# Kernel optimization log

Hardware: AMD Instinct MI355X
Metric: run time of the kernel (lower is better)

The kernel has to match this reference:

```python
import jax, jax.numpy as jnp
import numpy as np

B, S, D, DH = 4, 2048, 1024, 64


def setup_inputs() -> dict:
    key = jax.random.key(0)
    ks = jax.random.split(key, 7)
    x = jax.random.normal(ks[0], (B, S, D), dtype=jnp.float32)
    def w(k):
        return jax.random.normal(k, (D, DH), dtype=jnp.float32) / np.sqrt(D).astype(np.float32)
    return {
        'x': x,
        'w_q_u': w(ks[1]), 'w_k_u': w(ks[2]), 'w_v_u': w(ks[3]),
        'w_q_c': w(ks[4]), 'w_k_c': w(ks[5]), 'w_v_c': w(ks[6]),
    }


def reference(x, w_q_u, w_k_u, w_v_u, w_q_c, w_k_c, w_v_c):
    b, n, _ = x.shape
    scale = w_q_u.shape[-1] ** -0.5
    # projections (LinearNoBias -> plain matmul)
    Q_u = x @ w_q_u
    K_u = x @ w_k_u
    V_u = x @ w_v_u
    Q_c = x @ w_q_c
    K_c = x @ w_k_c
    V_c = x @ w_v_c

    i = jnp.arange(n)
    causal = i[:, None] >= i[None, :]        # True where j <= i (binary causal / keep for S_c)
    lookahead = i[:, None] < i[None, :]      # True where j > i (allowed in sigmoid term)

    # term1: [b, n, n], zeroed above the diagonal via binary causal mask
    term1 = jnp.einsum('bid,bjd->bij', Q_c, V_u) * scale * causal.astype(x.dtype)

    # sigmoid gate: lookahead mask adds -inf on/below the diagonal -> sigmoid = 0 there
    logits_u = jnp.einsum('bid,bjd->bij', Q_u, K_u) * scale
    sigmoid_term = jax.nn.sigmoid(jnp.where(lookahead, logits_u, -jnp.inf))

    # nested n^3 matmul: S_u[b,i,k] = sum_j term1[b,i,j] * sigmoid_term[b,k,j]
    S_u = jnp.einsum('bij,bkj->bik', term1, sigmoid_term)

    S_c = jnp.where(causal, jnp.einsum('bid,bjd->bij', Q_c, K_c) * scale, -jnp.inf)

    attn = jax.nn.softmax(S_c - jax.nn.silu(S_u), axis=-1)
    return jnp.einsum('bij,bjd->bid', attn, V_c)
```

## Files before the change

kernel.cpp:

```cpp
#include <hip/hip_runtime.h>
#include <hip/hip_bf16.h>

typedef short bf16x8 __attribute__((ext_vector_type(8)));
typedef float f32x4  __attribute__((ext_vector_type(4)));
typedef _Float16 f16x8 __attribute__((ext_vector_type(8)));

#define MFMA16(a,b,c)  __builtin_amdgcn_mfma_f32_16x16x32_bf16((a),(b),(c),0,0,0)
#define MFMAF16(a,b,c) __builtin_amdgcn_mfma_f32_16x16x32_f16((a),(b),(c),0,0,0)

#define GLDS16(g,l) __builtin_amdgcn_global_load_lds( \
    (const __attribute__((address_space(1))) void*)(g), \
    (__attribute__((address_space(3))) void*)(l), 16, 0, 0)

__device__ __forceinline__ short f2bf(float f){
  union { float f; unsigned u; } v; v.f = f;
  unsigned r = v.u + 0x7fffu + ((v.u >> 16) & 1u);
  return (short)(r >> 16);
}
__device__ __forceinline__ float bf2f(short h){
  union { unsigned u; float f; } v; v.u = ((unsigned)(unsigned short)h) << 16;
  return v.f;
}
__device__ __forceinline__ void split8v(f32x4 a, f32x4 b, bf16x8& h, bf16x8& l){
  float t[8] = {a[0],a[1],a[2],a[3],b[0],b[1],b[2],b[3]};
  #pragma unroll
  for (int e = 0; e < 8; ++e){
    short hs = f2bf(t[e]);
    h[e] = hs;
    l[e] = f2bf(t[e] - bf2f(hs));
  }
}

__global__ void k_prep(const float* w0, const float* w1, const float* w2,
                       const float* w3, const float* w4, const float* w5,
                       const float* __restrict__ x,
                       unsigned short* __restrict__ wth, unsigned short* __restrict__ wtl,
                       unsigned short* __restrict__ xh, unsigned short* __restrict__ xl){
  int gb = blockIdx.x;
  if (gb < 1536){
    int p = gb >> 8;
    const float* wp = p==0?w0:p==1?w1:p==2?w2:p==3?w3:p==4?w4:w5;
    int idx = (gb & 255)*256 + threadIdx.x;
    int n = idx >> 10, k = idx & 1023;
    float v = wp[k*64 + n];
    short hs = f2bf(v);
    wth[(size_t)p*65536 + n*1024 + k] = (unsigned short)hs;
    wtl[(size_t)p*65536 + n*1024 + k] = (unsigned short)f2bf(v - bf2f(hs));
  } else {
    size_t i = ((size_t)(gb - 1536)*256 + threadIdx.x)*8;
    f32x4 a = *(const f32x4*)(x + i);
    f32x4 b = *(const f32x4*)(x + i + 4);
    bf16x8 h, l;
    split8v(a, b, h, l);
    *(bf16x8*)(xh + i) = h;
    *(bf16x8*)(xl + i) = l;
  }
}

__global__ __launch_bounds__(256) void k_proj(
    const unsigned short* __restrict__ xh, const unsigned short* __restrict__ xl,
    const unsigned short* __restrict__ wth, const unsigned short* __restrict__ wtl,
    unsigned short* __restrict__ projh, unsigned short* __restrict__ projl,
    _Float16* __restrict__ vct, _Float16* __restrict__ vuth, _Float16* __restrict__ vutl){
  __shared__ __align__(16) char sm[49152];
  int blk = blockIdx.x;
  int rb = blk/3, pg = blk - rb*3;
  int tid = threadIdx.x, w = tid >> 6, lane = tid & 63;
  int lm = lane & 15, quad = lane >> 4;
  int srow = lane >> 3, scg = (lane & 7) ^ srow;
  const char* xhg = (const char*)xh;
  const char* xlg = (const char*)xl;
  const char* w0h = (const char*)wth + (size_t)(pg*2  )*131072;
  const char* w0l = (const char*)wtl + (size_t)(pg*2  )*131072;
  const char* w1h = (const char*)wth + (size_t)(pg*2+1)*131072;
  const char* w1l = (const char*)wtl + (size_t)(pg*2+1)*131072;
  f32x4 acc[2][4] = {};
  for (int k0 = 0; k0 < 1024; k0 += 64){
    __syncthreads();
    size_t cb = (size_t)k0*2 + scg*16;
    #pragma unroll
    for (int i2 = 0; i2 < 2; ++i2){
      int i = w*2 + i2;
      size_t gx = (size_t)(rb*64 + i*8 + srow)*2048 + cb;
      size_t gw = (size_t)(i*8 + srow)*2048 + cb;
      GLDS16(xhg + gx, sm +         i*1024);
      GLDS16(xlg + gx, sm +  8192 + i*1024);
      GLDS16(w0h + gw, sm + 16384 + i*1024);
      GLDS16(w0l + gw, sm + 24576 + i*1024);
      GLDS16(w1h + gw, sm + 32768 + i*1024);
      GLDS16(w1l + gw, sm + 40960 + i*1024);
    }
    __syncthreads();
    #pragma unroll
    for (int ks = 0; ks < 2; ++ks){
      int ra = w*16 + lm;
      int offa = ra*128 + (((ks*4+quad) ^ (ra&7))*16);
      bf16x8 ah = *(const bf16x8*)(sm + offa);
      bf16x8 al = *(const bf16x8*)(sm + 8192 + offa);
      #pragma unroll
      for (int sub = 0; sub < 2; ++sub){
        #pragma unroll
        for (int n = 0; n < 4; ++n){
          int r = n*16 + lm;
          int off = r*128 + (((ks*4+quad) ^ (r&7))*16);
          bf16x8 bh = *(const bf16x8*)(sm + 16384 + sub*16384 + off);
          bf16x8 bl = *(const bf16x8*)(sm + 24576 + sub*16384 + off);
          acc[sub][n] = MFMA16(ah, bh, acc[sub][n]);
          acc[sub][n] = MFMA16(ah, bl, acc[sub][n]);
          acc[sub][n] = MFMA16(al, bh, acc[sub][n]);
        }
      }
    }
  }
  #pragma unroll
  for (int sub = 0; sub < 2; ++sub){
    int p = pg*2 + sub;
    if (p != 5){
      unsigned short* oph = projh + (size_t)p*524288;
      unsigned short* opl = projl + (size_t)p*524288;
      #pragma unroll
      for (int n = 0; n < 4; ++n)
        #pragma unroll
        for (int e = 0; e < 4; ++e){
          int r = rb*64 + w*16 + quad*4 + e;
          float f = acc[sub][n][e];
          short hs = f2bf(f);
          oph[(size_t)r*64 + n*16 + lm] = (unsigned short)hs;
          opl[(size_t)r*64 + n*16 + lm] = (unsigned short)f2bf(f - bf2f(hs));
        }
    }
  }
  if (pg == 1 || pg == 2){
    int sub = (pg == 1) ? 0 : 1;
    float (*T)[65] = (float (*)[65])sm;
    __syncthreads();
    #pragma unroll
    for (int n = 0; n < 4; ++n)
      #pragma unroll
      for (int e = 0; e < 4; ++e)
        T[w*16 + quad*4 + e][n*16 + lm] = acc[sub][n][e];
    __syncthreads();
    int b2 = rb >> 5, sl = (rb & 31)*64;
    int d = tid >> 2, sp = (tid & 3)*16;
    size_t o = (size_t)b2*131072 + (size_t)d*2048 + sl + sp;
    if (sub == 1){
      f16x8 h0, h1;
      #pragma unroll
      for (int j = 0; j < 8; ++j) h0[j] = (_Float16)T[sp + j][d];
      #pragma unroll
      for (int j = 0; j < 8; ++j) h1[j] = (_Float16)T[sp + 8 + j][d];
      *(f16x8*)(vct + o) = h0; *(f16x8*)(vct + o + 8) = h1;
    } else {
      f16x8 h0, h1, l0, l1;
      #pragma unroll
      for (int j = 0; j < 8; ++j){
        float f = T[sp + j][d];
        _Float16 h = (_Float16)f;
        h0[j] = h; l0[j] = (_Float16)(f - (float)h);
      }
      #pragma unroll
      for (int j = 0; j < 8; ++j){
        float f = T[sp + 8 + j][d];
        _Float16 h = (_Float16)f;
        h1[j] = h; l1[j] = (_Float16)(f - (float)h);
      }
      *(f16x8*)(vuth + o) = h0; *(f16x8*)(vuth + o + 8) = h1;
      *(f16x8*)(vutl + o) = l0; *(f16x8*)(vutl + o + 8) = l1;
    }
  }
}

__global__ __launch_bounds__(256,3) void k_p2(
    const unsigned short* __restrict__ ph, const unsigned short* __restrict__ pl,
    const _Float16* __restrict__ vuth, const _Float16* __restrict__ vutl,
    _Float16* __restrict__ sg, _Float16* __restrict__ t1d, float* __restrict__ W){
  __shared__ __align__(16) char sm[32768];
  int b = blockIdx.y;
  int t = blockIdx.x;
  bool isSig = t < 136;
  int a = 0, bb = 0;
  if (isSig){
    #pragma unroll 1
    for (int aa = 0; aa < 16; ++aa){
      int c = 16 - aa;
      if (t < c){ a = aa; bb = aa + t; break; }
      t -= c;
    }
  } else {
    a = bb = t - 136;
  }
  int pa = isSig ? 0 : 3;
  int pb = isSig ? 1 : 2;
  const char* Ahg = (const char*)ph + (size_t)pa*1048576;
  const char* Alg = (const char*)pl + (size_t)pa*1048576;
  const char* Bhg = (const char*)ph + (size_t)pb*1048576;
  const char* Blg = (const char*)pl + (size_t)pb*1048576;
  int tid = threadIdx.x, w = tid >> 6, lane = tid & 63;
  int lm = lane & 15, quad = lane >> 4;
  int wm = (w & 1)*64, wn = (w >> 1)*64;
  f32x4 acc[4][4] = {};
  #pragma unroll
  for (int ks = 0; ks < 2; ++ks){
    bf16x8 bh[4], bl[4];
    #pragma unroll
    for (int n = 0; n < 4; ++n){
      size_t off = (size_t)(b*2048 + bb*128 + wn + n*16 + lm)*128 + (ks*32 + quad*8)*2;
      bh[n] = *(const bf16x8*)(Bhg + off);
      bl[n] = *(const bf16x8*)(Blg + off);
    }
    #pragma unroll
    for (int m = 0; m < 4; ++m){
      size_t off = (size_t)(b*2048 + a*128 + wm + m*16 + lm)*128 + (ks*32 + quad*8)*2;
      bf16x8 ah = *(const bf16x8*)(Ahg + off);
      bf16x8 al = *(const bf16x8*)(Alg + off);
      #pragma unroll
      for (int n = 0; n < 4; ++n){
        acc[m][n] = MFMA16(ah, bh[n], acc[m][n]);
        acc[m][n] = MFMA16(ah, bl[n], acc[m][n]);
        acc[m][n] = MFMA16(al, bh[n], acc[m][n]);
      }
    }
  }
  #pragma unroll
  for (int m = 0; m < 4; ++m){
    #pragma unroll
    for (int n = 0; n < 4; ++n){
      #pragma unroll
      for (int e = 0; e < 4; ++e){
        int il = wm + m*16 + quad*4 + e;
        int jl = wn + n*16 + lm;
        int gi = a*128 + il, gj = bb*128 + jl;
        float v = acc[m][n][e];
        float outv;
        if (isSig) outv = (gj >  gi) ? (1.0f/(1.0f + __expf(-v*0.125f))) : 0.0f;
        else       outv = (gj <= gi) ? v : 0.0f;
        *(_Float16*)(sm + ((il*256 + jl*2) ^ ((il & 7) << 4))) = (_Float16)outv;
      }
    }
  }
  __syncthreads();
  char* outp = isSig
    ? (char*)(sg + (size_t)b*4194304 + (size_t)(a*128)*2048 + bb*128)
    : (char*)t1d + (size_t)(b*16 + a)*32768;
  size_t rstride = isSig ? 4096 : 256;
  #pragma unroll
  for (int r = 0; r < 8; ++r){
    int lrow = w*32 + r*4 + (lane >> 4);
    int c16 = lane & 15;
    f32x4 vv = *(const f32x4*)(sm + ((lrow*256 + c16*16) ^ ((lrow & 7) << 4)));
    *(f32x4*)(outp + (size_t)lrow*rstride + c16*16) = vv;
  }
  if (isSig){
    int wm2 = (w & 1)*64, wn2 = (w >> 1)*32;
    f32x4 acc2[4][2] = {};
    #pragma unroll
    for (int ks = 0; ks < 4; ++ks){
      f16x8 bh2[2], bl2[2];
      #pragma unroll
      for (int n = 0; n < 2; ++n){
        int d = wn2 + n*16 + lm;
        size_t jo = ((size_t)(b*64 + d)*2048 + bb*128 + ks*32 + quad*8)*2;
        bh2[n] = *(const f16x8*)((const char*)vuth + jo);
        bl2[n] = *(const f16x8*)((const char*)vutl + jo);
      }
      #pragma unroll
      for (int m = 0; m < 4; ++m){
        int k = wm2 + m*16 + lm;
        f16x8 af = *(const f16x8*)(sm + ((k*256 + ks*64 + quad*16) ^ ((k & 7) << 4)));
        #pragma unroll
        for (int n = 0; n < 2; ++n){
          acc2[m][n] = MFMAF16(af, bh2[n], acc2[m][n]);
          acc2[m][n] = MFMAF16(af, bl2[n], acc2[m][n]);
        }
      }
    }
    float* Wp = W + (size_t)(b*136 + bb*(bb+1)/2 + a)*8192;
    #pragma unroll
    for (int m = 0; m < 4; ++m)
      #pragma unroll
      for (int n = 0; n < 2; ++n)
        #pragma unroll
        for (int e = 0; e < 4; ++e){
          int r = wm2 + m*16 + quad*4 + e;
          int col = wn2 + n*16 + lm;
          Wp[r*64 + col] = acc2[m][n][e];
        }
  }
}

__global__ __launch_bounds__(256) void k_scan(const float* __restrict__ W,
    unsigned short* __restrict__ Ph, unsigned short* __restrict__ Pl){
  int g = blockIdx.x, b = blockIdx.y;
  int ck = g >> 2, ksub = g & 3;
  if (ck >= 15) return;
  int tid = threadIdx.x;
  int rl = ksub*32 + (tid >> 3);
  int col = (tid & 7)*8;
  float acc[8] = {};
  #pragma unroll 1
  for (int c = ck; c < 15; ++c){
    const float* wt = W + (size_t)(b*136 + c*(c+1)/2 + ck)*8192 + rl*64 + col;
    f32x4 v0 = *(const f32x4*)wt;
    f32x4 v1 = *(const f32x4*)(wt + 4);
    #pragma unroll
    for (int e = 0; e < 4; ++e){ acc[e] += v0[e]; acc[4+e] += v1[e]; }
    size_t o = ((size_t)(b*16 + c + 1)*2048 + ck*128 + rl)*64 + col;
    bf16x8 h, l;
    #pragma unroll
    for (int e = 0; e < 8; ++e){
      short hs = f2bf(acc[e]);
      h[e] = hs;
      l[e] = f2bf(acc[e] - bf2f(hs));
    }
    *(bf16x8*)(Ph + o) = h;
    *(bf16x8*)(Pl + o) = l;
  }
}

__global__ __launch_bounds__(256,2) void k_p3(
    const unsigned short* __restrict__ ph, const unsigned short* __restrict__ pl,
    const _Float16* __restrict__ t1d, const _Float16* __restrict__ sg,
    const unsigned short* __restrict__ Ph, const unsigned short* __restrict__ Pl,
    _Float16* __restrict__ lg){
  __shared__ __align__(16) char sm[32768];
  int t0 = blockIdx.x, b = blockIdx.y;
  int t = (t0 & 7)*17 + (t0 >> 3);
  int ci = 0, ck = 0;
  #pragma unroll 1
  for (int aa = 0; aa < 16; ++aa){
    if (t < aa + 1){ ci = aa; ck = t; break; }
    t -= aa + 1;
  }
  int tid = threadIdx.x, w = tid >> 6, lane = tid & 63;
  int lm = lane & 15, quad = lane >> 4;
  int wm = (w & 1)*64, wn = (w >> 1)*64;
  f32x4 su[4][4] = {}, sc[4][4] = {};
  bool hasP = (ck < ci);

  const char* Qh = (const char*)ph + (size_t)3*1048576;
  const char* Ql = (const char*)pl + (size_t)3*1048576;
  const char* Kh = (const char*)ph + (size_t)4*1048576;
  const char* Kl = (const char*)pl + (size_t)4*1048576;

  #pragma unroll
  for (int ks = 0; ks < 2; ++ks){
    bf16x8 kh[4], kl[4], bh[4], bl[4];
    #pragma unroll
    for (int n = 0; n < 4; ++n){
      size_t offk = (size_t)(b*2048 + ck*128 + wn + n*16 + lm)*128 + (ks*32 + quad*8)*2;
      kh[n] = *(const bf16x8*)(Kh + offk);
      kl[n] = *(const bf16x8*)(Kl + offk);
    }
    if (hasP){
      #pragma unroll
      for (int n = 0; n < 4; ++n){
        size_t offp = (((size_t)(b*16 + ci)*2048 + ck*128 + wn + n*16 + lm)*64 + ks*32 + quad*8)*2;
        bh[n] = *(const bf16x8*)((const char*)Ph + offp);
        bl[n] = *(const bf16x8*)((const char*)Pl + offp);
      }
    }
    #pragma unroll
    for (int m = 0; m < 4; ++m){
      size_t offq = (size_t)(b*2048 + ci*128 + wm + m*16 + lm)*128 + (ks*32 + quad*8)*2;
      bf16x8 ah = *(const bf16x8*)(Qh + offq);
      bf16x8 al = *(const bf16x8*)(Ql + offq);
      #pragma unroll
      for (int n = 0; n < 4; ++n){
        sc[m][n] = MFMA16(ah, kh[n], sc[m][n]);
        sc[m][n] = MFMA16(ah, kl[n], sc[m][n]);
        sc[m][n] = MFMA16(al, kh[n], sc[m][n]);
      }
      if (hasP){
        #pragma unroll
        for (int n = 0; n < 4; ++n){
          su[m][n] = MFMA16(ah, bh[n], su[m][n]);
          su[m][n] = MFMA16(ah, bl[n], su[m][n]);
          su[m][n] = MFMA16(al, bh[n], su[m][n]);
        }
      }
    }
  }
  const char* t1b = (const char*)t1d + (size_t)(b*16 + ci)*32768;
  const char* sgb = (const char*)sg + (size_t)b*8388608;
  #pragma unroll
  for (int ks = 0; ks < 4; ++ks){
    f16x8 bs[4];
    #pragma unroll
    for (int n = 0; n < 4; ++n)
      bs[n] = *(const f16x8*)(sgb + ((size_t)(ck*128 + wn + n*16 + lm)*2048 + ci*128 + ks*32 + quad*8)*2);
    #pragma unroll
    for (int m = 0; m < 4; ++m){
      f16x8 at = *(const f16x8*)(t1b + ((wm + m*16 + lm)*128 + ks*32 + quad*8)*2);
      #pragma unroll
      for (int n = 0; n < 4; ++n)
        su[m][n] = MFMAF16(at, bs[n], su[m][n]);
    }
  }
  _Float16* Tt = (_Float16*)sm;
  #pragma unroll
  for (int m = 0; m < 4; ++m)
    #pragma unroll
    for (int n = 0; n < 4; ++n)
      #pragma unroll
      for (int e = 0; e < 4; ++e){
        int il = wm + m*16 + quad*4 + e;
        int jl = wn + n*16 + lm;
        float xv = 0.125f*su[m][n][e];
        float sg1 = 1.0f/(1.0f + __expf(-xv));
        Tt[il*128 + jl] = (_Float16)(sc[m][n][e]*0.125f - xv*sg1);
      }
  __syncthreads();
  _Float16* lgb = lg + (size_t)b*4194304;
  #pragma unroll
  for (int r = 0; r < 8; ++r){
    int lrow = w*32 + r*4 + (lane >> 4);
    int c16 = lane & 15;
    f32x4 vv = *(const f32x4*)(sm + lrow*256 + c16*16);
    *(f32x4*)((char*)(lgb + (size_t)(ci*128 + lrow)*2048 + ck*128) + c16*16) = vv;
  }
}

__global__ __launch_bounds__(256,2) void k_p4(const _Float16* __restrict__ lg,
    const _Float16* __restrict__ vct, float* __restrict__ out){
  __shared__ __align__(16) char sm[66048];
  float* Mz = (float*)(sm + 65536);
  float* Sz = (float*)(sm + 65792);
  int b = blockIdx.y;
  int b1 = blockIdx.x;
  int tid = threadIdx.x, w = tid >> 6, lane = tid & 63;
  int lm = lane & 15, quad = lane >> 4;
  const _Float16* vb = vct + (size_t)b*131072;
  for (int pass = 0; pass < 2; ++pass){
    int band = pass ? (127 - b1) : b1;
    int r0 = band*16;
    const char* lgb = (const char*)lg + ((size_t)b*4194304 + (size_t)r0*2048)*2;
    int nkt = ((r0 + 15) >> 6) + 1;
    int fc = (r0 + 1) >> 6;
    int srl = lane >> 3, ssl = lane & 7;
    __syncthreads();
    for (int kt = w; kt < nkt; kt += 4){
      #pragma unroll
      for (int i2 = 0; i2 < 2; ++i2){
        int rl = i2*8 + srl;
        GLDS16(lgb + (size_t)rl*4096 + kt*128 + ((ssl ^ (rl & 7))*16),
               sm + kt*2048 + i2*1024);
      }
    }
    __syncthreads();
    float m_r = -3.0e38f;
    for (int kt = w; kt < nkt; kt += 4){
      #pragma unroll
      for (int half = 0; half < 2; ++half){
        int sl = quad*2 + half;
        f16x8 v = *(const f16x8*)(sm + kt*2048 + lm*128 + ((sl ^ (lm & 7))*16));
        int cb = kt*64 + sl*8;
        #pragma unroll
        for (int e = 0; e < 8; ++e)
          m_r = (cb + e <= r0 + lm) ? fmaxf(m_r, (float)v[e]) : m_r;
      }
    }
    m_r = fmaxf(m_r, __shfl_xor(m_r, 16));
    m_r = fmaxf(m_r, __shfl_xor(m_r, 32));
    Mz[w*16 + lm] = m_r;
    __syncthreads();
    float mfin = fmaxf(fmaxf(Mz[lm], Mz[16 + lm]), fmaxf(Mz[32 + lm], Mz[48 + lm]));
    float s_r = 0.0f;
    for (int kt = w; kt < nkt; kt += 4){
      #pragma unroll
      for (int half = 0; half < 2; ++half){
        int sl = quad*2 + half;
        f16x8 v = *(const f16x8*)(sm + kt*2048 + lm*128 + ((sl ^ (lm & 7))*16));
        int cb = kt*64 + sl*8;
        #pragma unroll
        for (int e = 0; e < 8; ++e)
          if (cb + e <= r0 + lm) s_r += __expf((float)v[e] - mfin);
      }
    }
    s_r += __shfl_xor(s_r, 16);
    s_r += __shfl_xor(s_r, 32);
    Sz[w*16 + lm] = s_r;
    f32x4 acc[4] = {};
    for (int kt = w; kt < nkt; kt += 4){
      bool full = kt < fc;
      #pragma unroll
      for (int ks = 0; ks < 2; ++ks){
        f16x8 Lv = *(const f16x8*)(sm + kt*2048 + lm*128 + (((ks*4+quad) ^ (lm & 7))*16));
        int jbase = kt*64 + ks*32 + quad*8;
        f16x8 af;
        #pragma unroll
        for (int e = 0; e < 8; ++e){
          float p = __expf((float)Lv[e] - mfin);
          if (!full && (jbase + e > r0 + lm)) p = 0.0f;
          af[e] = (_Float16)p;
        }
        #pragma unroll
        for (int n = 0; n < 4; ++n){
          f16x8 bv = *(const f16x8*)(vb + (size_t)(n*16 + lm)*2048 + jbase);
          acc[n] = MFMAF16(af, bv, acc[n]);
        }
      }
    }
    __syncthreads();
    float* Ot = (float*)sm;
    #pragma unroll
    for (int n = 0; n < 4; ++n)
      #pragma unroll
      for (int e = 0; e < 4; ++e)
        Ot[(w*16 + quad*4 + e)*64 + n*16 + lm] = acc[n][e];
    __syncthreads();
    int row = tid >> 4, c4 = (tid & 15)*4;
    f32x4 s = *(const f32x4*)&Ot[row*64 + c4];
    #pragma unroll
    for (int ww = 1; ww < 4; ++ww){
      f32x4 t2 = *(const f32x4*)&Ot[(ww*16 + row)*64 + c4];
      s[0]+=t2[0]; s[1]+=t2[1]; s[2]+=t2[2]; s[3]+=t2[3];
    }
    float z = Sz[row] + Sz[16 + row] + Sz[32 + row] + Sz[48 + row];
    f32x4 o = { s[0]/z, s[1]/z, s[2]/z, s[3]/z };
    *(f32x4*)(out + ((size_t)b*2048 + r0 + row)*64 + c4) = o;
  }
}

static const size_t OFF_WTH   = 4194304;
static const size_t OFF_WTL   = 4980736;
static const size_t OFF_PROJH = 5767168;
static const size_t OFF_PROJL = 12058624;
static const size_t OFF_VCT   = 18350080;
static const size_t OFF_SG    = 19398656;
static const size_t OFF_LG    = 52953088;
static const size_t OFF_T1D   = 86507520;
static const size_t OFF_PH    = 88604672;
static const size_t OFF_PL    = 105381888;
static const size_t OFF_VUTH  = 122159104;
static const size_t OFF_VUTL  = 123207680;
static const size_t OFF_XH    = 124256256;
static const size_t OFF_XL    = 141033472;
static const size_t OFF_W     = OFF_XH;

extern "C" void kernel_launch(void* const* d_in, const int* in_sizes, int n_in,
                              void* d_out, int out_size, void* d_ws, size_t ws_size,
                              hipStream_t stream){
  (void)in_sizes; (void)n_in; (void)out_size; (void)ws_size;
  const float* x = (const float*)d_in[0];
  char* ws = (char*)d_ws;
  unsigned short* wth   = (unsigned short*)(ws + OFF_WTH);
  unsigned short* wtl   = (unsigned short*)(ws + OFF_WTL);
  unsigned short* projh = (unsigned short*)(ws + OFF_PROJH);
  unsigned short* projl = (unsigned short*)(ws + OFF_PROJL);
  _Float16*       vct   = (_Float16*)(ws + OFF_VCT);
  _Float16*       sg    = (_Float16*)(ws + OFF_SG);
  _Float16*       lg    = (_Float16*)(ws + OFF_LG);
  _Float16*       t1d   = (_Float16*)(ws + OFF_T1D);
  unsigned short* Phb   = (unsigned short*)(ws + OFF_PH);
  unsigned short* Plb   = (unsigned short*)(ws + OFF_PL);
  _Float16*       vuth  = (_Float16*)(ws + OFF_VUTH);
  _Float16*       vutl  = (_Float16*)(ws + OFF_VUTL);
  unsigned short* xh    = (unsigned short*)(ws + OFF_XH);
  unsigned short* xl    = (unsigned short*)(ws + OFF_XL);
  float*          Wb    = (float*)(ws + OFF_W);

  k_prep  <<<dim3(5632),   256, 0, stream>>>((const float*)d_in[1], (const float*)d_in[2],
                                             (const float*)d_in[3], (const float*)d_in[4],
                                             (const float*)d_in[5], (const float*)d_in[6],
                                             x, wth, wtl, xh, xl);
  k_proj  <<<dim3(384),    256, 0, stream>>>(xh, xl, wth, wtl, projh, projl, vct, vuth, vutl);
  k_p2    <<<dim3(152,4),  256, 0, stream>>>(projh, projl, vuth, vutl, sg, t1d, Wb);
  k_scan  <<<dim3(64,4),   256, 0, stream>>>(Wb, Phb, Plb);
  k_p3    <<<dim3(136,4),  256, 0, stream>>>(projh, projl, t1d, sg, Phb, Plb, lg);
  k_p4    <<<dim3(64,4),   256, 0, stream>>>(lg, vct, (float*)d_out);
}
```

Before: 207.3 us.

## Fuse logits tile computation with online-softmax PV into one kernel

Merges the logits-tile kernel and the softmax·V kernel into one kernel. Each block owns a 128-row query chunk and loops over key chunks, keeping a running max and sum (online softmax) and accumulating the output in registers. This removes the global fp16 logits buffer write and re-read and one launch. In exchange, parallelism drops to 64 blocks with a sequential per-block loop and triangular load imbalance.

```diff
diff --git a/kernel.cpp b/kernel.cpp
--- a/kernel.cpp
+++ b/kernel.cpp
@@ -317,208 +317,172 @@
   }
 }
 
-__global__ __launch_bounds__(256,2) void k_p3(
+__global__ __launch_bounds__(256,1) void k_fuse(
     const unsigned short* __restrict__ ph, const unsigned short* __restrict__ pl,
     const _Float16* __restrict__ t1d, const _Float16* __restrict__ sg,
     const unsigned short* __restrict__ Ph, const unsigned short* __restrict__ Pl,
-    _Float16* __restrict__ lg){
+    const _Float16* __restrict__ vct, float* __restrict__ out){
   __shared__ __align__(16) char sm[32768];
-  int t0 = blockIdx.x, b = blockIdx.y;
-  int t = (t0 & 7)*17 + (t0 >> 3);
-  int ci = 0, ck = 0;
-  #pragma unroll 1
-  for (int aa = 0; aa < 16; ++aa){
-    if (t < aa + 1){ ci = aa; ck = t; break; }
-    t -= aa + 1;
-  }
+  __shared__ float Mld[128], M2s[2][128], Fz[128], S2[128];
+  int ci = blockIdx.x, b = blockIdx.y;
   int tid = threadIdx.x, w = tid >> 6, lane = tid & 63;
   int lm = lane & 15, quad = lane >> 4;
   int wm = (w & 1)*64, wn = (w >> 1)*64;
-  f32x4 su[4][4] = {}, sc[4][4] = {};
-  bool hasP = (ck < ci);
 
   const char* Qh = (const char*)ph + (size_t)3*1048576;
   const char* Ql = (const char*)pl + (size_t)3*1048576;
   const char* Kh = (const char*)ph + (size_t)4*1048576;
   const char* Kl = (const char*)pl + (size_t)4*1048576;
-
-  #pragma unroll
-  for (int ks = 0; ks < 2; ++ks){
-    bf16x8 kh[4], kl[4], bh[4], bl[4];
-    #pragma unroll
-    for (int n = 0; n < 4; ++n){
-      size_t offk = (size_t)(b*2048 + ck*128 + wn + n*16 + lm)*128 + (ks*32 + quad*8)*2;
-      kh[n] = *(const bf16x8*)(Kh + offk);
-      kl[n] = *(const bf16x8*)(Kl + offk);
-    }
-    if (hasP){
-      #pragma unroll
-      for (int n = 0; n < 4; ++n){
-        size_t offp = (((size_t)(b*16 + ci)*2048 + ck*128 + wn + n*16 + lm)*64 + ks*32 + quad*8)*2;
-        bh[n] = *(const bf16x8*)((const char*)Ph + offp);
-        bl[n] = *(const bf16x8*)((const char*)Pl + offp);
-      }
-    }
-    #pragma unroll
-    for (int m = 0; m < 4; ++m){
-      size_t offq = (size_t)(b*2048 + ci*128 + wm + m*16 + lm)*128 + (ks*32 + quad*8)*2;
-      bf16x8 ah = *(const bf16x8*)(Qh + offq);
-      bf16x8 al = *(const bf16x8*)(Ql + offq);
-      #pragma unroll
-      for (int n = 0; n < 4; ++n){
-        sc[m][n] = MFMA16(ah, kh[n], sc[m][n]);
-        sc[m][n] = MFMA16(ah, kl[n], sc[m][n]);
-        sc[m][n] = MFMA16(al, kh[n], sc[m][n]);
-      }
-      if (hasP){
-        #pragma unroll
-        for (int n = 0; n < 4; ++n){
-          su[m][n] = MFMA16(ah, bh[n], su[m][n]);
-          su[m][n] = MFMA16(ah, bl[n], su[m][n]);
-          su[m][n] = MFMA16(al, bh[n], su[m][n]);
-        }
-      }
-    }
-  }
   const char* t1b = (const char*)t1d + (size_t)(b*16 + ci)*32768;
   const char* sgb = (const char*)sg + (size_t)b*8388608;
+  const _Float16* vb = vct + (size_t)b*131072;
+
+  float m_r = -3.0e38f, l_r = 0.0f;
+  f32x4 Ov[2][4] = {};
+
+  for (int ck = 0; ck <= ci; ++ck){
+    f32x4 su[4][4] = {}, sc[4][4] = {};
+    bool hasP = (ck < ci);
+    #pragma unroll
+    for (int ks = 0; ks < 2; ++ks){
+      bf16x8 kh[4], kl[4], bh[4], bl[4];
+      #pragma unroll
+      for (int n = 0; n < 4; ++n){
+        size_t offk = (size_t)(b*2048 + ck*128 + wn + n*16 + lm)*128 + (ks*32 + quad*8)*2;
+        kh[n] = *(const bf16x8*)(Kh + offk);
+        kl[n] = *(const bf16x8*)(Kl + offk);
+      }
+      if (hasP){
+        #pragma unroll
+        for (int n = 0; n < 4; ++n){
+          size_t offp = (((size_t)(b*16 + ci)*2048 + ck*128 + wn + n*16 + lm)*64 + ks*32 + quad*8)*2;
+          bh[n] = *(const bf16x8*)((const char*)Ph + offp);
+          bl[n] = *(const bf16x8*)((const char*)Pl + offp);
+        }
+      }
+      #pragma unroll
+      for (int m = 0; m < 4; ++m){
+        size_t offq = (size_t)(b*2048 + ci*128 + wm + m*16 + lm)*128 + (ks*32 + quad*8)*2;
+        bf16x8 ah = *(const bf16x8*)(Qh + offq);
+        bf16x8 al = *(const bf16x8*)(Ql + offq);
+        #pragma unroll
+        for (int n = 0; n < 4; ++n){
+          sc[m][n] = MFMA16(ah, kh[n], sc[m][n]);
+          sc[m][n] = MFMA16(ah, kl[n], sc[m][n]);
+          sc[m][n] = MFMA16(al, kh[n], sc[m][n]);
+        }
+        if (hasP){
+          #pragma unroll
+          for (int n = 0; n < 4; ++n){
+            su[m][n] = MFMA16(ah, bh[n], su[m][n]);
+            su[m][n] = MFMA16(ah, bl[n], su[m][n]);
+            su[m][n] = MFMA16(al, bh[n], su[m][n]);
+          }
+        }
+      }
+    }
+    #pragma unroll
+    for (int ks = 0; ks < 4; ++ks){
+      f16x8 bs[4];
+      #pragma unroll
+      for (int n = 0; n < 4; ++n)
+        bs[n] = *(const f16x8*)(sgb + ((size_t)(ck*128 + wn + n*16 + lm)*2048 + ci*128 + ks*32 + quad*8)*2);
+      #pragma unroll
+      for (int m = 0; m < 4; ++m){
+        f16x8 at = *(const f16x8*)(t1b + ((wm + m*16 + lm)*128 + ks*32 + quad*8)*2);
+        #pragma unroll
+        for (int n = 0; n < 4; ++n)
+          su[m][n] = MFMAF16(at, bs[n], su[m][n]);
+      }
+    }
+    bool diag = (ck == ci);
+    #pragma unroll
+    for (int m = 0; m < 4; ++m){
+      f32x4 hm = { -3.0e38f, -3.0e38f, -3.0e38f, -3.0e38f };
+      #pragma unroll
+      for (int n = 0; n < 4; ++n){
+        #pragma unroll
+        for (int e = 0; e < 4; ++e){
+          int il = wm + m*16 + quad*4 + e;
+          int jl = wn + n*16 + lm;
+          float xv = 0.125f*su[m][n][e];
+          float sg1 = 1.0f/(1.0f + __expf(-xv));
+          float val = sc[m][n][e]*0.125f - xv*sg1;
+          bool keep = !diag || (jl <= il);
+          *(_Float16*)(sm + ((il*256 + jl*2) ^ ((il & 7) << 4))) =
+              keep ? (_Float16)val : (_Float16)(-65504.0f);
+          if (keep) hm[e] = fmaxf(hm[e], val);
+        }
+      }
+      #pragma unroll
+      for (int e = 0; e < 4; ++e){
+        float v = hm[e];
+        v = fmaxf(v, __shfl_xor(v, 1));
+        v = fmaxf(v, __shfl_xor(v, 2));
+        v = fmaxf(v, __shfl_xor(v, 4));
+        v = fmaxf(v, __shfl_xor(v, 8));
+        if (lm == 0) M2s[wn >> 6][wm + m*16 + quad*4 + e] = v;
+      }
+    }
+    __syncthreads();
+    if (tid < 128){
+      float mnew = fmaxf(m_r, fmaxf(M2s[0][tid], M2s[1][tid]));
+      Fz[tid] = __expf(m_r - mnew);
+      m_r = mnew;
+      Mld[tid] = mnew;
+    }
+    __syncthreads();
+    #pragma unroll
+    for (int m2 = 0; m2 < 2; ++m2)
+      #pragma unroll
+      for (int e = 0; e < 4; ++e){
+        float f = Fz[w*32 + m2*16 + quad*4 + e];
+        #pragma unroll
+        for (int n = 0; n < 4; ++n) Ov[m2][n][e] *= f;
+      }
+    float mr0 = Mld[w*32 + lm], mr1 = Mld[w*32 + 16 + lm];
+    float s0 = 0.0f, s1 = 0.0f;
+    #pragma unroll
+    for (int ks = 0; ks < 4; ++ks){
+      f16x8 bv[4];
+      #pragma unroll
+      for (int n = 0; n < 4; ++n)
+        bv[n] = *(const f16x8*)(vb + (size_t)(n*16 + lm)*2048 + ck*128 + ks*32 + quad*8);
+      #pragma unroll
+      for (int m2 = 0; m2 < 2; ++m2){
+        int r = w*32 + m2*16 + lm;
+        f16x8 Lv = *(const f16x8*)(sm + ((r*256 + ks*64 + quad*16) ^ ((r & 7) << 4)));
+        float mrr = m2 ? mr1 : mr0;
+        f16x8 af;
+        #pragma unroll
+        for (int e = 0; e < 8; ++e){
+          float p = __expf((float)Lv[e] - mrr);
+          if (m2) s1 += p; else s0 += p;
+          af[e] = (_Float16)p;
+        }
+        #pragma unroll
+        for (int n = 0; n < 4; ++n)
+          Ov[m2][n] = MFMAF16(af, bv[n], Ov[m2][n]);
+      }
+    }
+    s0 += __shfl_xor(s0, 16); s0 += __shfl_xor(s0, 32);
+    s1 += __shfl_xor(s1, 16); s1 += __shfl_xor(s1, 32);
+    if (quad == 0){ S2[w*32 + lm] = s0; S2[w*32 + 16 + lm] = s1; }
+    __syncthreads();
+    if (tid < 128) l_r = l_r * Fz[tid] + S2[tid];
+  }
+  if (tid < 128) S2[tid] = l_r;
+  __syncthreads();
   #pragma unroll
-  for (int ks = 0; ks < 4; ++ks){
-    f16x8 bs[4];
-    #pragma unroll
-    for (int n = 0; n < 4; ++n)
-      bs[n] = *(const f16x8*)(sgb + ((size_t)(ck*128 + wn + n*16 + lm)*2048 + ci*128 + ks*32 + quad*8)*2);
-    #pragma unroll
-    for (int m = 0; m < 4; ++m){
-      f16x8 at = *(const f16x8*)(t1b + ((wm + m*16 + lm)*128 + ks*32 + quad*8)*2);
+  for (int m2 = 0; m2 < 2; ++m2)
+    #pragma unroll
+    for (int e = 0; e < 4; ++e){
+      int r = w*32 + m2*16 + quad*4 + e;
+      float z = S2[r];
       #pragma unroll
       for (int n = 0; n < 4; ++n)
-        su[m][n] = MFMAF16(at, bs[n], su[m][n]);
-    }
-  }
-  _Float16* Tt = (_Float16*)sm;
-  #pragma unroll
-  for (int m = 0; m < 4; ++m)
-    #pragma unroll
-    for (int n = 0; n < 4; ++n)
-      #pragma unroll
-      for (int e = 0; e < 4; ++e){
-        int il = wm + m*16 + quad*4 + e;
-        int jl = wn + n*16 + lm;
-        float xv = 0.125f*su[m][n][e];
-        float sg1 = 1.0f/(1.0f + __expf(-xv));
-        Tt[il*128 + jl] = (_Float16)(sc[m][n][e]*0.125f - xv*sg1);
-      }
-  __syncthreads();
-  _Float16* lgb = lg + (size_t)b*4194304;
-  #pragma unroll
-  for (int r = 0; r < 8; ++r){
-    int lrow = w*32 + r*4 + (lane >> 4);
-    int c16 = lane & 15;
-    f32x4 vv = *(const f32x4*)(sm + lrow*256 + c16*16);
-    *(f32x4*)((char*)(lgb + (size_t)(ci*128 + lrow)*2048 + ck*128) + c16*16) = vv;
-  }
-}
-
-__global__ __launch_bounds__(256,2) void k_p4(const _Float16* __restrict__ lg,
-    const _Float16* __restrict__ vct, float* __restrict__ out){
-  __shared__ __align__(16) char sm[66048];
-  float* Mz = (float*)(sm + 65536);
-  float* Sz = (float*)(sm + 65792);
-  int b = blockIdx.y;
-  int b1 = blockIdx.x;
-  int tid = threadIdx.x, w = tid >> 6, lane = tid & 63;
-  int lm = lane & 15, quad = lane >> 4;
-  const _Float16* vb = vct + (size_t)b*131072;
-  for (int pass = 0; pass < 2; ++pass){
-    int band = pass ? (127 - b1) : b1;
-    int r0 = band*16;
-    const char* lgb = (const char*)lg + ((size_t)b*4194304 + (size_t)r0*2048)*2;
-    int nkt = ((r0 + 15) >> 6) + 1;
-    int fc = (r0 + 1) >> 6;
-    int srl = lane >> 3, ssl = lane & 7;
-    __syncthreads();
-    for (int kt = w; kt < nkt; kt += 4){
-      #pragma unroll
-      for (int i2 = 0; i2 < 2; ++i2){
-        int rl = i2*8 + srl;
-        GLDS16(lgb + (size_t)rl*4096 + kt*128 + ((ssl ^ (rl & 7))*16),
-               sm + kt*2048 + i2*1024);
-      }
-    }
-    __syncthreads();
-    float m_r = -3.0e38f;
-    for (int kt = w; kt < nkt; kt += 4){
-      #pragma unroll
-      for (int half = 0; half < 2; ++half){
-        int sl = quad*2 + half;
-        f16x8 v = *(const f16x8*)(sm + kt*2048 + lm*128 + ((sl ^ (lm & 7))*16));
-        int cb = kt*64 + sl*8;
-        #pragma unroll
-        for (int e = 0; e < 8; ++e)
-          m_r = (cb + e <= r0 + lm) ? fmaxf(m_r, (float)v[e]) : m_r;
-      }
-    }
-    m_r = fmaxf(m_r, __shfl_xor(m_r, 16));
-    m_r = fmaxf(m_r, __shfl_xor(m_r, 32));
-    Mz[w*16 + lm] = m_r;
-    __syncthreads();
-    float mfin = fmaxf(fmaxf(Mz[lm], Mz[16 + lm]), fmaxf(Mz[32 + lm], Mz[48 + lm]));
-    float s_r = 0.0f;
-    for (int kt = w; kt < nkt; kt += 4){
-      #pragma unroll
-      for (int half = 0; half < 2; ++half){
-        int sl = quad*2 + half;
-        f16x8 v = *(const f16x8*)(sm + kt*2048 + lm*128 + ((sl ^ (lm & 7))*16));
-        int cb = kt*64 + sl*8;
-        #pragma unroll
-        for (int e = 0; e < 8; ++e)
-          if (cb + e <= r0 + lm) s_r += __expf((float)v[e] - mfin);
-      }
-    }
-    s_r += __shfl_xor(s_r, 16);
-    s_r += __shfl_xor(s_r, 32);
-    Sz[w*16 + lm] = s_r;
-    f32x4 acc[4] = {};
-    for (int kt = w; kt < nkt; kt += 4){
-      bool full = kt < fc;
-      #pragma unroll
-      for (int ks = 0; ks < 2; ++ks){
-        f16x8 Lv = *(const f16x8*)(sm + kt*2048 + lm*128 + (((ks*4+quad) ^ (lm & 7))*16));
-        int jbase = kt*64 + ks*32 + quad*8;
-        f16x8 af;
-        #pragma unroll
-        for (int e = 0; e < 8; ++e){
-          float p = __expf((float)Lv[e] - mfin);
-          if (!full && (jbase + e > r0 + lm)) p = 0.0f;
-          af[e] = (_Float16)p;
-        }
-        #pragma unroll
-        for (int n = 0; n < 4; ++n){
-          f16x8 bv = *(const f16x8*)(vb + (size_t)(n*16 + lm)*2048 + jbase);
-          acc[n] = MFMAF16(af, bv, acc[n]);
-        }
-      }
-    }
-    __syncthreads();
-    float* Ot = (float*)sm;
-    #pragma unroll
-    for (int n = 0; n < 4; ++n)
-      #pragma unroll
-      for (int e = 0; e < 4; ++e)
-        Ot[(w*16 + quad*4 + e)*64 + n*16 + lm] = acc[n][e];
-    __syncthreads();
-    int row = tid >> 4, c4 = (tid & 15)*4;
-    f32x4 s = *(const f32x4*)&Ot[row*64 + c4];
-    #pragma unroll
-    for (int ww = 1; ww < 4; ++ww){
-      f32x4 t2 = *(const f32x4*)&Ot[(ww*16 + row)*64 + c4];
-      s[0]+=t2[0]; s[1]+=t2[1]; s[2]+=t2[2]; s[3]+=t2[3];
-    }
-    float z = Sz[row] + Sz[16 + row] + Sz[32 + row] + Sz[48 + row];
-    f32x4 o = { s[0]/z, s[1]/z, s[2]/z, s[3]/z };
-    *(f32x4*)(out + ((size_t)b*2048 + r0 + row)*64 + c4) = o;
-  }
+        out[((size_t)b*2048 + ci*128 + r)*64 + n*16 + lm] = Ov[m2][n][e] / z;
+    }
 }
 
 static const size_t OFF_WTH   = 4194304;
@@ -527,7 +491,6 @@
 static const size_t OFF_PROJL = 12058624;
 static const size_t OFF_VCT   = 18350080;
 static const size_t OFF_SG    = 19398656;
-static const size_t OFF_LG    = 52953088;
 static const size_t OFF_T1D   = 86507520;
 static const size_t OFF_PH    = 88604672;
 static const size_t OFF_PL    = 105381888;
@@ -549,7 +512,6 @@
   unsigned short* projl = (unsigned short*)(ws + OFF_PROJL);
   _Float16*       vct   = (_Float16*)(ws + OFF_VCT);
   _Float16*       sg    = (_Float16*)(ws + OFF_SG);
-  _Float16*       lg    = (_Float16*)(ws + OFF_LG);
   _Float16*       t1d   = (_Float16*)(ws + OFF_T1D);
   unsigned short* Phb   = (unsigned short*)(ws + OFF_PH);
   unsigned short* Plb   = (unsigned short*)(ws + OFF_PL);
@@ -566,6 +528,5 @@
   k_proj  <<<dim3(384),    256, 0, stream>>>(xh, xl, wth, wtl, projh, projl, vct, vuth, vutl);
   k_p2    <<<dim3(152,4),  256, 0, stream>>>(projh, projl, vuth, vutl, sg, t1d, Wb);
   k_scan  <<<dim3(64,4),   256, 0, stream>>>(Wb, Phb, Plb);
-  k_p3    <<<dim3(136,4),  256, 0, stream>>>(projh, projl, t1d, sg, Phb, Plb, lg);
-  k_p4    <<<dim3(64,4),   256, 0, stream>>>(lg, vct, (float*)d_out);
-}
+  k_fuse  <<<dim3(16,4),   256, 0, stream>>>(projh, projl, t1d, sg, Phb, Plb, vct, (float*)d_out);
+}
```

Measured after the change: 394.8 us. +90.5%, slower.
